# Kernel tuning notes

Hardware: AMD Instinct MI355X
Metric: run time of the kernel (lower is better)

Reference implementation:

```python
import jax, jax.numpy as jnp
import numpy as np

S, B, IN, H, DFF, OUT, L, NHEAD, WINDOW = 2048, 4, 64, 1024, 1024, 64, 3, 4, 4
EPS = 1e-5


def _layer_norm(x, scale, bias):
    m = jnp.mean(x, axis=-1, keepdims=True)
    v = jnp.var(x, axis=-1, keepdims=True)
    return (x - m) * jax.lax.rsqrt(v + EPS) * scale + bias


def setup_inputs() -> dict:
    key = jax.random.key(0)
    ks = jax.random.split(key, 12)
    s = 0.02
    return {
        "src": jax.random.normal(ks[0], (S, B, IN), dtype=jnp.float32),
        "Wenc": jax.random.normal(ks[1], (H, IN), dtype=jnp.float32) * s,
        "benc": jnp.zeros((H,), jnp.float32),
        "Wqkv": jax.random.normal(ks[2], (L, 3 * H, H), dtype=jnp.float32) * s,
        "bqkv": jnp.zeros((L, 3 * H), jnp.float32),
        "Wo": jax.random.normal(ks[3], (L, H, H), dtype=jnp.float32) * s,
        "bo": jnp.zeros((L, H), jnp.float32),
        "W1": jax.random.normal(ks[4], (L, DFF, H), dtype=jnp.float32) * s,
        "b1": jnp.zeros((L, DFF), jnp.float32),
        "W2": jax.random.normal(ks[5], (L, H, DFF), dtype=jnp.float32) * s,
        "b2": jnp.zeros((L, H), jnp.float32),
        "ln1_s": jnp.ones((L, H), jnp.float32),
        "ln1_b": jnp.zeros((L, H), jnp.float32),
        "ln2_s": jnp.ones((L, H), jnp.float32),
        "ln2_b": jnp.zeros((L, H), jnp.float32),
        "Wout": jax.random.normal(ks[6], (OUT, H), dtype=jnp.float32) * s,
        "bout": jnp.zeros((OUT,), jnp.float32),
    }


def _banded_mask(sz):
    # triu(1) masked + lower-band (j < i-4) masked => allowed: i-4 <= j <= i
    i = jnp.arange(sz)[:, None]
    j = jnp.arange(sz)[None, :]
    allowed = (j <= i) & (j >= i - WINDOW)
    return jnp.where(allowed, 0.0, -1e9).astype(jnp.float32)


def reference(src, Wenc, benc, Wqkv, bqkv, Wo, bo, W1, b1, W2, b2,
              ln1_s, ln1_b, ln2_s, ln2_b, Wout, bout):
    dh = H // NHEAD
    mask = _banded_mask(src.shape[0])  # [S, S]
    x = src @ Wenc.T + benc  # [S, B, H]  (NOTE: pos_encoder is never applied in the source)

    def layer(x, p):
        Wqkv_, bqkv_, Wo_, bo_, W1_, b1_, W2_, b2_, s1, g1, s2, g2 = p
        qkv = x @ Wqkv_.T + bqkv_  # [S, B, 3H]
        q, k, v = jnp.split(qkv, 3, axis=-1)
        sS, sB = x.shape[0], x.shape[1]
        q = q.reshape(sS, sB, NHEAD, dh)
        k = k.reshape(sS, sB, NHEAD, dh)
        v = v.reshape(sS, sB, NHEAD, dh)
        scores = jnp.einsum('sbhd,tbhd->bhst', q, k) / jnp.sqrt(jnp.float32(dh))
        scores = scores + mask  # broadcast over [b, h]
        attn = jax.nn.softmax(scores, axis=-1)
        ctx = jnp.einsum('bhst,tbhd->sbhd', attn, v).reshape(sS, sB, H)
        attn_out = ctx @ Wo_.T + bo_
        x = _layer_norm(x + attn_out, s1, g1)  # post-norm (PyTorch default)
        ff = jax.nn.relu(x @ W1_.T + b1_) @ W2_.T + b2_
        x = _layer_norm(x + ff, s2, g2)
        return x, None

    x, _ = jax.lax.scan(layer, x, (Wqkv, bqkv, Wo, bo, W1, b1, W2, b2,
                                   ln1_s, ln1_b, ln2_s, ln2_b))
    return x @ Wout.T + bout  # [S, B, OUT]
```

## Files before the change

### kernel.cpp

```cpp
#include <hip/hip_runtime.h>
#include <hip/hip_bf16.h>

#define S_LEN   2048
#define BATCH   4
#define IN_DIM  64
#define H_DIM   1024
#define DFF_DIM 1024
#define OUT_DIM 64
#define NLAYER  3
#define NHEADS  4
#define DHEAD   256
#define WIN     4
#define ROWS    (S_LEN*BATCH)
#define QKV_LD  (3*H_DIM)


typedef __bf16 bf16x8 __attribute__((ext_vector_type(8)));
typedef float  f32x4  __attribute__((ext_vector_type(4)));

__device__ __forceinline__ float bfbits2f(unsigned int u) {
  union { unsigned int i; float f; } c; c.i = u << 16; return c.f;
}
__device__ __forceinline__ unsigned short f2bfbits(float f) {
  __hip_bfloat16 h = __float2bfloat16(f);
  return __builtin_bit_cast(unsigned short, h);
}

__device__ __forceinline__ void g2l16(const void* g, void* l) {
  __builtin_amdgcn_global_load_lds((__attribute__((address_space(1))) void*)g,
                                   (__attribute__((address_space(3))) void*)l,
                                   16, 0, 0);
}

__global__ __launch_bounds__(256)
void cvt_k(const float* __restrict__ in, __hip_bfloat16* __restrict__ out, int n)
{
  int i = (blockIdx.x * 256 + threadIdx.x) * 4;
  if (i >= n) return;
  float4 v = *(const float4*)(in + i);
  uint2 o;
  o.x = (unsigned)f2bfbits(v.x) | ((unsigned)f2bfbits(v.y) << 16);
  o.y = (unsigned)f2bfbits(v.z) | ((unsigned)f2bfbits(v.w) << 16);
  *(uint2*)(out + i) = o;
}

template<int RELU, int OUTF32, int ADDRES>
__global__ __launch_bounds__(256, 2)
void gemm_bt(const __hip_bfloat16* __restrict__ A, int lda,
             const __hip_bfloat16* __restrict__ B,
             const float* __restrict__ bias,
             void* __restrict__ Cp, int ldc,
             const __hip_bfloat16* __restrict__ R, int ldr,
             int M, int N, int K)
{
  __shared__ __align__(16) __hip_bfloat16 As[128 * 32];
  __shared__ __align__(16) __hip_bfloat16 Bs[128 * 32];

  const int tid  = threadIdx.x;
  const int lane = tid & 63;
  const int wave = tid >> 6;
  const int quad = lane >> 4;
  const int l16  = lane & 15;
  const int m0 = blockIdx.y * 128;
  const int n0 = blockIdx.x * 128;
  const int wr = (wave >> 1) * 64;
  const int wc = (wave & 1) * 64;

  const int p0  = wave * 64 + lane;
  const int p1  = p0 + 256;
  const int ar0 = p0 >> 2, ac0 = (((p0 & 3) ^ ((ar0 >> 1) & 3))) * 8;
  const int ar1 = p1 >> 2, ac1 = (((p1 & 3) ^ ((ar1 >> 1) & 3))) * 8;
  const int br0 = min(n0 + ar0, N - 1);
  const int br1 = min(n0 + ar1, N - 1);
  __hip_bfloat16* lA0 = &As[(wave * 64)       * 8];
  __hip_bfloat16* lA1 = &As[(wave * 64 + 256) * 8];
  __hip_bfloat16* lB0 = &Bs[(wave * 64)       * 8];
  __hip_bfloat16* lB1 = &Bs[(wave * 64 + 256) * 8];

  f32x4 acc[4][4] = {};

  for (int k0 = 0; k0 < K; k0 += 32) {
    g2l16(A + (size_t)(m0 + ar0) * lda + k0 + ac0, lA0);
    g2l16(A + (size_t)(m0 + ar1) * lda + k0 + ac1, lA1);
    g2l16(B + (size_t)br0 * K + k0 + ac0, lB0);
    g2l16(B + (size_t)br1 * K + k0 + ac1, lB1);
    __syncthreads();

    bf16x8 af[4], bfr[4];
#pragma unroll
    for (int i = 0; i < 4; i++) {
      const int row = wr + i * 16 + l16;
      af[i] = *(const bf16x8*)&As[row * 32 + ((quad ^ ((row >> 1) & 3)) * 8)];
    }
#pragma unroll
    for (int j = 0; j < 4; j++) {
      const int row = wc + j * 16 + l16;
      bfr[j] = *(const bf16x8*)&Bs[row * 32 + ((quad ^ ((row >> 1) & 3)) * 8)];
    }
#pragma unroll
    for (int i = 0; i < 4; i++)
#pragma unroll
      for (int j = 0; j < 4; j++)
        acc[i][j] = __builtin_amdgcn_mfma_f32_16x16x32_bf16(af[i], bfr[j], acc[i][j], 0, 0, 0);
    __syncthreads();
  }

#pragma unroll
  for (int j = 0; j < 4; j++) {
    int col = n0 + wc + j * 16 + l16;
    if (col < N) {
      float bv = bias[col];
#pragma unroll
      for (int i = 0; i < 4; i++) {
        int row = m0 + wr + i * 16 + quad * 4;
#pragma unroll
        for (int r = 0; r < 4; r++) {
          float v = acc[i][j][r] + bv;
          if (RELU) v = fmaxf(v, 0.f);
          if (ADDRES) v += __bfloat162float(R[(size_t)(row + r) * ldr + col]);
          if (OUTF32) ((float*)Cp)[(size_t)(row + r) * ldc + col] = v;
          else ((__hip_bfloat16*)Cp)[(size_t)(row + r) * ldc + col] = __float2bfloat16(v);
        }
      }
    }
  }
}

__global__ __launch_bounds__(256)
void attn_k(__hip_bfloat16* __restrict__ qkv)
{
  __shared__ __align__(16) __hip_bfloat16 Ks[68 * 256];
  __shared__ __align__(16) __hip_bfloat16 Vs[68 * 256];

  const int s0 = blockIdx.x * 64;
  const int b  = blockIdx.y >> 2;
  const int h  = blockIdx.y & 3;
  const int tid  = threadIdx.x;
  const int wave = tid >> 6;
  const int lane = tid & 63;
  const size_t hbase = (size_t)h * DHEAD;

  for (int c = tid; c < 68 * 32; c += 256) {
    const int row  = c >> 5;
    const int col8 = (c & 31) * 8;
    const int gs = s0 - 4 + row;
    if (gs >= 0) {
      const size_t gbase = (size_t)(gs * BATCH + b) * QKV_LD + hbase + col8;
      *(uint4*)&Ks[row * 256 + col8] = *(const uint4*)(qkv + gbase + H_DIM);
      *(uint4*)&Vs[row * 256 + col8] = *(const uint4*)(qkv + gbase + 2 * H_DIM);
    }
  }
  __syncthreads();

  for (int qi = 0; qi < 16; qi++) {
    const int s  = s0 + wave * 16 + qi;
    const int lr = wave * 16 + qi;
    const size_t qoff = (size_t)(s * BATCH + b) * QKV_LD + hbase + (lane << 2);

    float q0, q1, q2, q3;
    {
      uint2 t = *(const uint2*)(qkv + qoff);
      q0 = bfbits2f(t.x & 0xffff); q1 = bfbits2f(t.x >> 16);
      q2 = bfbits2f(t.y & 0xffff); q3 = bfbits2f(t.y >> 16);
    }

    float sc[WIN + 1];
#pragma unroll
    for (int jj = 0; jj <= WIN; jj++) {
      float v = -1e30f;
      if (s - WIN + jj >= 0) {
        uint2 t = *(const uint2*)&Ks[(lr + jj) * 256 + (lane << 2)];
        float p = q0 * bfbits2f(t.x & 0xffff) + q1 * bfbits2f(t.x >> 16)
                + q2 * bfbits2f(t.y & 0xffff) + q3 * bfbits2f(t.y >> 16);
#pragma unroll
        for (int o = 32; o; o >>= 1) p += __shfl_xor(p, o);
        v = p * 0.0625f;
      }
      sc[jj] = v;
    }

    float mx = sc[0];
#pragma unroll
    for (int jj = 1; jj <= WIN; jj++) mx = fmaxf(mx, sc[jj]);
    float p[WIN + 1], den = 0.f;
#pragma unroll
    for (int jj = 0; jj <= WIN; jj++) { p[jj] = __expf(sc[jj] - mx); den += p[jj]; }

    float a0 = 0.f, a1 = 0.f, a2 = 0.f, a3 = 0.f;
#pragma unroll
    for (int jj = 0; jj <= WIN; jj++) {
      if (s - WIN + jj >= 0) {
        uint2 t = *(const uint2*)&Vs[(lr + jj) * 256 + (lane << 2)];
        a0 += p[jj] * bfbits2f(t.x & 0xffff); a1 += p[jj] * bfbits2f(t.x >> 16);
        a2 += p[jj] * bfbits2f(t.y & 0xffff); a3 += p[jj] * bfbits2f(t.y >> 16);
      }
    }
    const float rl = 1.f / den;
    uint2 o;
    o.x = (unsigned)f2bfbits(a0 * rl) | ((unsigned)f2bfbits(a1 * rl) << 16);
    o.y = (unsigned)f2bfbits(a2 * rl) | ((unsigned)f2bfbits(a3 * rl) << 16);
    *(uint2*)(qkv + qoff) = o;
  }
}

__global__ __launch_bounds__(256)
void ln_k(const __hip_bfloat16* __restrict__ y, int ys,
          const float* __restrict__ g, const float* __restrict__ be,
          __hip_bfloat16* __restrict__ xout)
{
  const int row = blockIdx.x, tid = threadIdx.x;
  uint2 yv = *(const uint2*)(y + (size_t)row * ys + tid * 4);
  float t0 = bfbits2f(yv.x & 0xffff);
  float t1 = bfbits2f(yv.x >> 16);
  float t2 = bfbits2f(yv.y & 0xffff);
  float t3 = bfbits2f(yv.y >> 16);
  float s  = t0 + t1 + t2 + t3;
  float ss = t0 * t0 + t1 * t1 + t2 * t2 + t3 * t3;
#pragma unroll
  for (int o = 32; o; o >>= 1) { s += __shfl_down(s, o); ss += __shfl_down(ss, o); }
  __shared__ float rs[4], rss[4];
  if ((tid & 63) == 0) { rs[tid >> 6] = s; rss[tid >> 6] = ss; }
  __syncthreads();
  float S  = rs[0] + rs[1] + rs[2] + rs[3];
  float SS = rss[0] + rss[1] + rss[2] + rss[3];
  const float inv = 1.f / (float)H_DIM;
  float mean = S * inv;
  float var  = SS * inv - mean * mean;
  float rstd = rsqrtf(var + 1e-5f);
  float4 gv = *(const float4*)(g + tid * 4);
  float4 bv = *(const float4*)(be + tid * 4);
  float o0 = (t0 - mean) * rstd * gv.x + bv.x;
  float o1 = (t1 - mean) * rstd * gv.y + bv.y;
  float o2 = (t2 - mean) * rstd * gv.z + bv.z;
  float o3 = (t3 - mean) * rstd * gv.w + bv.w;
  uint2 ob;
  ob.x = (unsigned)f2bfbits(o0) | ((unsigned)f2bfbits(o1) << 16);
  ob.y = (unsigned)f2bfbits(o2) | ((unsigned)f2bfbits(o3) << 16);
  *(uint2*)(xout + (size_t)row * H_DIM + tid * 4) = ob;
}

extern "C" void kernel_launch(void* const* d_in, const int* in_sizes, int n_in,
                              void* d_out, int out_size, void* d_ws, size_t ws_size,
                              hipStream_t stream) {
  const float* src   = (const float*)d_in[0];
  const float* Wenc  = (const float*)d_in[1];
  const float* benc  = (const float*)d_in[2];
  const float* Wqkv  = (const float*)d_in[3];
  const float* bqkv  = (const float*)d_in[4];
  const float* Wo    = (const float*)d_in[5];
  const float* bo    = (const float*)d_in[6];
  const float* W1    = (const float*)d_in[7];
  const float* b1    = (const float*)d_in[8];
  const float* W2    = (const float*)d_in[9];
  const float* b2    = (const float*)d_in[10];
  const float* ln1s  = (const float*)d_in[11];
  const float* ln1b  = (const float*)d_in[12];
  const float* ln2s  = (const float*)d_in[13];
  const float* ln2b  = (const float*)d_in[14];
  const float* Wout  = (const float*)d_in[15];
  const float* bout  = (const float*)d_in[16];

  char* ws = (char*)d_ws;
  __hip_bfloat16* WB   = (__hip_bfloat16*)ws;
  __hip_bfloat16* srcb = WB;
  __hip_bfloat16* wenc = WB + 524288;
  __hip_bfloat16* wqkv = WB + 589824;
  __hip_bfloat16* wo   = WB + 10027008;
  __hip_bfloat16* w1   = WB + 13172736;
  __hip_bfloat16* w2   = WB + 16318464;
  __hip_bfloat16* wout = WB + 19464192;
  __hip_bfloat16* xb  = (__hip_bfloat16*)(ws + (size_t)40 * 1048576);
  __hip_bfloat16* qkv = (__hip_bfloat16*)(ws + (size_t)56 * 1048576);
  __hip_bfloat16* ctxp = qkv;
  __hip_bfloat16* ybuf = qkv + H_DIM;
  __hip_bfloat16* hbuf = qkv + 2 * H_DIM;

  const dim3 blk(256);
  #define CVT(inp, outp, n) cvt_k<<<dim3(((n) / 4 + 255) / 256), blk, 0, stream>>>(inp, outp, n)

  CVT(src,  srcb, 524288);
  CVT(Wenc, wenc, 65536);
  CVT(Wqkv, wqkv, 9437184);
  CVT(Wo,   wo,   3145728);
  CVT(W1,   w1,   3145728);
  CVT(W2,   w2,   3145728);
  CVT(Wout, wout, 65536);

  gemm_bt<0, 0, 0><<<dim3(H_DIM / 128, ROWS / 128), blk, 0, stream>>>(
      srcb, IN_DIM, wenc, benc, xb, H_DIM, nullptr, 0, ROWS, H_DIM, IN_DIM);

  for (int l = 0; l < NLAYER; l++) {
    gemm_bt<0, 0, 0><<<dim3(QKV_LD / 128, ROWS / 128), blk, 0, stream>>>(
        xb, H_DIM, wqkv + (size_t)l * QKV_LD * H_DIM, bqkv + l * QKV_LD,
        qkv, QKV_LD, nullptr, 0, ROWS, QKV_LD, H_DIM);
    attn_k<<<dim3(S_LEN / 64, BATCH * NHEADS), blk, 0, stream>>>(qkv);
    gemm_bt<0, 0, 1><<<dim3(H_DIM / 128, ROWS / 128), blk, 0, stream>>>(
        ctxp, QKV_LD, wo + (size_t)l * H_DIM * H_DIM, bo + l * H_DIM,
        ybuf, QKV_LD, xb, H_DIM, ROWS, H_DIM, H_DIM);
    ln_k<<<dim3(ROWS), blk, 0, stream>>>(ybuf, QKV_LD, ln1s + l * H_DIM, ln1b + l * H_DIM, xb);
    gemm_bt<1, 0, 0><<<dim3(DFF_DIM / 128, ROWS / 128), blk, 0, stream>>>(
        xb, H_DIM, w1 + (size_t)l * DFF_DIM * H_DIM, b1 + l * DFF_DIM,
        hbuf, QKV_LD, nullptr, 0, ROWS, DFF_DIM, H_DIM);
    gemm_bt<0, 0, 1><<<dim3(H_DIM / 128, ROWS / 128), blk, 0, stream>>>(
        hbuf, QKV_LD, w2 + (size_t)l * H_DIM * DFF_DIM, b2 + l * H_DIM,
        ybuf, QKV_LD, xb, H_DIM, ROWS, H_DIM, DFF_DIM);
    ln_k<<<dim3(ROWS), blk, 0, stream>>>(ybuf, QKV_LD, ln2s + l * H_DIM, ln2b + l * H_DIM, xb);
  }

  gemm_bt<0, 1, 0><<<dim3(1, ROWS / 128), blk, 0, stream>>>(
      xb, H_DIM, wout, bout, d_out, OUT_DIM, nullptr, 0, ROWS, OUT_DIM, H_DIM);
}
```

Baseline: 857.7 us.

## Double GEMM K-tile to 64 and map attention to one wave per query-head

The bf16 MFMA GEMM now stages 64-wide K slices in shared memory instead of 32, with a new 8-way XOR swizzle, and runs two MFMA sub-steps per barrier pair. This halves the number of loop iterations and __syncthreads calls. The cost is double the LDS per block (32 KB), which may limit occupancy. The banded attention kernel drops its shared-memory K/V staging: each wave handles one (position, batch, head) and reads its five K/V rows straight from global memory. That gives far more parallelism, but relies on cache hits for the rows that neighbouring waves re-read.

```diff
diff --git a/kernel.cpp b/kernel.cpp
--- a/kernel.cpp
+++ b/kernel.cpp
@@ -53,8 +53,8 @@
              const __hip_bfloat16* __restrict__ R, int ldr,
              int M, int N, int K)
 {
-  __shared__ __align__(16) __hip_bfloat16 As[128 * 32];
-  __shared__ __align__(16) __hip_bfloat16 Bs[128 * 32];
+  __shared__ __align__(16) __hip_bfloat16 As[128 * 64];
+  __shared__ __align__(16) __hip_bfloat16 Bs[128 * 64];
 
   const int tid  = threadIdx.x;
   const int lane = tid & 63;
@@ -66,42 +66,49 @@
   const int wr = (wave >> 1) * 64;
   const int wc = (wave & 1) * 64;
 
-  const int p0  = wave * 64 + lane;
-  const int p1  = p0 + 256;
-  const int ar0 = p0 >> 2, ac0 = (((p0 & 3) ^ ((ar0 >> 1) & 3))) * 8;
-  const int ar1 = p1 >> 2, ac1 = (((p1 & 3) ^ ((ar1 >> 1) & 3))) * 8;
-  const int br0 = min(n0 + ar0, N - 1);
-  const int br1 = min(n0 + ar1, N - 1);
-  __hip_bfloat16* lA0 = &As[(wave * 64)       * 8];
-  __hip_bfloat16* lA1 = &As[(wave * 64 + 256) * 8];
-  __hip_bfloat16* lB0 = &Bs[(wave * 64)       * 8];
-  __hip_bfloat16* lB1 = &Bs[(wave * 64 + 256) * 8];
+  int arow[4], acol[4], brow[4];
+#pragma unroll
+  for (int s = 0; s < 4; s++) {
+    const int p = tid + (s << 8);
+    arow[s] = p >> 3;
+    acol[s] = ((p & 7) ^ ((p >> 3) & 7)) * 8;
+    brow[s] = min(n0 + arow[s], N - 1);
+  }
 
   f32x4 acc[4][4] = {};
-
-  for (int k0 = 0; k0 < K; k0 += 32) {
-    g2l16(A + (size_t)(m0 + ar0) * lda + k0 + ac0, lA0);
-    g2l16(A + (size_t)(m0 + ar1) * lda + k0 + ac1, lA1);
-    g2l16(B + (size_t)br0 * K + k0 + ac0, lB0);
-    g2l16(B + (size_t)br1 * K + k0 + ac1, lB1);
+  const int nk = K >> 6;
+
+  for (int t = 0; t < nk; ++t) {
+    const int k0 = t << 6;
+#pragma unroll
+    for (int s = 0; s < 4; s++) {
+      const int lo = (wave * 64 + (s << 8)) * 8;
+      g2l16(A + (size_t)(m0 + arow[s]) * lda + k0 + acol[s], &As[lo]);
+      g2l16(B + (size_t)brow[s] * K + k0 + acol[s], &Bs[lo]);
+    }
     __syncthreads();
 
-    bf16x8 af[4], bfr[4];
-#pragma unroll
-    for (int i = 0; i < 4; i++) {
-      const int row = wr + i * 16 + l16;
-      af[i] = *(const bf16x8*)&As[row * 32 + ((quad ^ ((row >> 1) & 3)) * 8)];
-    }
-#pragma unroll
-    for (int j = 0; j < 4; j++) {
-      const int row = wc + j * 16 + l16;
-      bfr[j] = *(const bf16x8*)&Bs[row * 32 + ((quad ^ ((row >> 1) & 3)) * 8)];
-    }
-#pragma unroll
-    for (int i = 0; i < 4; i++)
-#pragma unroll
-      for (int j = 0; j < 4; j++)
-        acc[i][j] = __builtin_amdgcn_mfma_f32_16x16x32_bf16(af[i], bfr[j], acc[i][j], 0, 0, 0);
+#pragma unroll
+    for (int kh = 0; kh < 2; kh++) {
+      bf16x8 af[4], bfr[4];
+#pragma unroll
+      for (int i = 0; i < 4; i++) {
+        const int row = wr + i * 16 + l16;
+        const int c   = (kh * 4 + quad) ^ (row & 7);
+        af[i] = *(const bf16x8*)&As[row * 64 + c * 8];
+      }
+#pragma unroll
+      for (int j = 0; j < 4; j++) {
+        const int row = wc + j * 16 + l16;
+        const int c   = (kh * 4 + quad) ^ (row & 7);
+        bfr[j] = *(const bf16x8*)&Bs[row * 64 + c * 8];
+      }
+#pragma unroll
+      for (int i = 0; i < 4; i++)
+#pragma unroll
+        for (int j = 0; j < 4; j++)
+          acc[i][j] = __builtin_amdgcn_mfma_f32_16x16x32_bf16(af[i], bfr[j], acc[i][j], 0, 0, 0);
+    }
     __syncthreads();
   }
 
@@ -129,78 +136,58 @@
 __global__ __launch_bounds__(256)
 void attn_k(__hip_bfloat16* __restrict__ qkv)
 {
-  __shared__ __align__(16) __hip_bfloat16 Ks[68 * 256];
-  __shared__ __align__(16) __hip_bfloat16 Vs[68 * 256];
-
-  const int s0 = blockIdx.x * 64;
-  const int b  = blockIdx.y >> 2;
-  const int h  = blockIdx.y & 3;
-  const int tid  = threadIdx.x;
-  const int wave = tid >> 6;
-  const int lane = tid & 63;
-  const size_t hbase = (size_t)h * DHEAD;
-
-  for (int c = tid; c < 68 * 32; c += 256) {
-    const int row  = c >> 5;
-    const int col8 = (c & 31) * 8;
-    const int gs = s0 - 4 + row;
-    if (gs >= 0) {
-      const size_t gbase = (size_t)(gs * BATCH + b) * QKV_LD + hbase + col8;
-      *(uint4*)&Ks[row * 256 + col8] = *(const uint4*)(qkv + gbase + H_DIM);
-      *(uint4*)&Vs[row * 256 + col8] = *(const uint4*)(qkv + gbase + 2 * H_DIM);
-    }
-  }
-  __syncthreads();
-
-  for (int qi = 0; qi < 16; qi++) {
-    const int s  = s0 + wave * 16 + qi;
-    const int lr = wave * 16 + qi;
-    const size_t qoff = (size_t)(s * BATCH + b) * QKV_LD + hbase + (lane << 2);
-
-    float q0, q1, q2, q3;
-    {
-      uint2 t = *(const uint2*)(qkv + qoff);
-      q0 = bfbits2f(t.x & 0xffff); q1 = bfbits2f(t.x >> 16);
-      q2 = bfbits2f(t.y & 0xffff); q3 = bfbits2f(t.y >> 16);
-    }
-
-    float sc[WIN + 1];
-#pragma unroll
-    for (int jj = 0; jj <= WIN; jj++) {
-      float v = -1e30f;
-      if (s - WIN + jj >= 0) {
-        uint2 t = *(const uint2*)&Ks[(lr + jj) * 256 + (lane << 2)];
-        float p = q0 * bfbits2f(t.x & 0xffff) + q1 * bfbits2f(t.x >> 16)
-                + q2 * bfbits2f(t.y & 0xffff) + q3 * bfbits2f(t.y >> 16);
-#pragma unroll
-        for (int o = 32; o; o >>= 1) p += __shfl_xor(p, o);
-        v = p * 0.0625f;
-      }
-      sc[jj] = v;
-    }
-
-    float mx = sc[0];
-#pragma unroll
-    for (int jj = 1; jj <= WIN; jj++) mx = fmaxf(mx, sc[jj]);
-    float p[WIN + 1], den = 0.f;
-#pragma unroll
-    for (int jj = 0; jj <= WIN; jj++) { p[jj] = __expf(sc[jj] - mx); den += p[jj]; }
-
-    float a0 = 0.f, a1 = 0.f, a2 = 0.f, a3 = 0.f;
-#pragma unroll
-    for (int jj = 0; jj <= WIN; jj++) {
-      if (s - WIN + jj >= 0) {
-        uint2 t = *(const uint2*)&Vs[(lr + jj) * 256 + (lane << 2)];
-        a0 += p[jj] * bfbits2f(t.x & 0xffff); a1 += p[jj] * bfbits2f(t.x >> 16);
-        a2 += p[jj] * bfbits2f(t.y & 0xffff); a3 += p[jj] * bfbits2f(t.y >> 16);
-      }
-    }
-    const float rl = 1.f / den;
-    uint2 o;
-    o.x = (unsigned)f2bfbits(a0 * rl) | ((unsigned)f2bfbits(a1 * rl) << 16);
-    o.y = (unsigned)f2bfbits(a2 * rl) | ((unsigned)f2bfbits(a3 * rl) << 16);
-    *(uint2*)(qkv + qoff) = o;
-  }
+  const int gw   = (blockIdx.x << 2) + (threadIdx.x >> 6);
+  const int lane = threadIdx.x & 63;
+  const int h = gw & (NHEADS - 1);
+  const int b = (gw >> 2) & (BATCH - 1);
+  const int s = gw >> 4;
+  const size_t hoff = (size_t)h * DHEAD + (lane << 2);
+
+  float q0, q1, q2, q3;
+  {
+    uint2 t = *(const uint2*)(qkv + (size_t)(s * BATCH + b) * QKV_LD + hoff);
+    q0 = bfbits2f(t.x & 0xffff); q1 = bfbits2f(t.x >> 16);
+    q2 = bfbits2f(t.y & 0xffff); q3 = bfbits2f(t.y >> 16);
+  }
+
+  float sc[WIN + 1];
+#pragma unroll
+  for (int jj = 0; jj <= WIN; jj++) {
+    int j = s - WIN + jj;
+    float v = -1e30f;
+    if (j >= 0) {
+      uint2 t = *(const uint2*)(qkv + (size_t)(j * BATCH + b) * QKV_LD + H_DIM + hoff);
+      float p = q0 * bfbits2f(t.x & 0xffff) + q1 * bfbits2f(t.x >> 16)
+              + q2 * bfbits2f(t.y & 0xffff) + q3 * bfbits2f(t.y >> 16);
+#pragma unroll
+      for (int o = 32; o; o >>= 1) p += __shfl_xor(p, o);
+      v = p * 0.0625f;
+    }
+    sc[jj] = v;
+  }
+
+  float mx = sc[0];
+#pragma unroll
+  for (int jj = 1; jj <= WIN; jj++) mx = fmaxf(mx, sc[jj]);
+  float p[WIN + 1], den = 0.f;
+#pragma unroll
+  for (int jj = 0; jj <= WIN; jj++) { p[jj] = __expf(sc[jj] - mx); den += p[jj]; }
+
+  float a0 = 0.f, a1 = 0.f, a2 = 0.f, a3 = 0.f;
+#pragma unroll
+  for (int jj = 0; jj <= WIN; jj++) {
+    int j = s - WIN + jj;
+    if (j >= 0) {
+      uint2 t = *(const uint2*)(qkv + (size_t)(j * BATCH + b) * QKV_LD + 2 * H_DIM + hoff);
+      a0 += p[jj] * bfbits2f(t.x & 0xffff); a1 += p[jj] * bfbits2f(t.x >> 16);
+      a2 += p[jj] * bfbits2f(t.y & 0xffff); a3 += p[jj] * bfbits2f(t.y >> 16);
+    }
+  }
+  float rl = 1.f / den;
+  uint2 o;
+  o.x = (unsigned)f2bfbits(a0 * rl) | ((unsigned)f2bfbits(a1 * rl) << 16);
+  o.y = (unsigned)f2bfbits(a2 * rl) | ((unsigned)f2bfbits(a3 * rl) << 16);
+  *(uint2*)(qkv + (size_t)(s * BATCH + b) * QKV_LD + hoff) = o;
 }
 
 __global__ __launch_bounds__(256)
@@ -293,7 +280,7 @@
     gemm_bt<0, 0, 0><<<dim3(QKV_LD / 128, ROWS / 128), blk, 0, stream>>>(
         xb, H_DIM, wqkv + (size_t)l * QKV_LD * H_DIM, bqkv + l * QKV_LD,
         qkv, QKV_LD, nullptr, 0, ROWS, QKV_LD, H_DIM);
-    attn_k<<<dim3(S_LEN / 64, BATCH * NHEADS), blk, 0, stream>>>(qkv);
+    attn_k<<<dim3(ROWS * NHEADS / 4), blk, 0, stream>>>(qkv);
     gemm_bt<0, 0, 1><<<dim3(H_DIM / 128, ROWS / 128), blk, 0, stream>>>(
         ctxp, QKV_LD, wo + (size_t)l * H_DIM * H_DIM, bo + l * H_DIM,
         ybuf, QKV_LD, xb, H_DIM, ROWS, H_DIM, H_DIM);
```

After: 737.5 us. -14.0%, faster.
